# Performance work log

Hardware: AMD Instinct MI355X
Metric: run time of the kernel (lower is better)

Reference implementation:

```python
import jax, jax.numpy as jnp
import numpy as np

PATCH = 7
PAD = PATCH // 2  # 3


def _to_gray(x):
    # x: [B,3,H,W] -> [B,1,H,W]
    return 0.299 * x[:, 0:1] + 0.587 * x[:, 1:2] + 0.114 * x[:, 2:3]


def _census_transform(x):
    # x: [B,C,H,W] RGB -> grayscale, then 48 shifted binary comparisons.
    if x.shape[1] == 3:
        x = _to_gray(x)
    B, C, H, W = x.shape
    x_pad = jnp.pad(x, ((0, 0), (0, 0), (PAD, PAD), (PAD, PAD)), mode='reflect')
    center = x
    feats = []
    for i in range(PATCH):
        for j in range(PATCH):
            if i == PAD and j == PAD:
                continue
            neighbor = x_pad[:, :, i:i + H, j:j + W]
            feats.append((center > neighbor).astype(x.dtype))
    return jnp.concatenate(feats, axis=1)  # [B,48,H,W]


def setup_inputs() -> dict:
    key = jax.random.key(0)
    k1, k2 = jax.random.split(key)
    B, C, H, W = 8, 3, 512, 512
    pred = jax.random.uniform(k1, (B, C, H, W), dtype=jnp.float32)
    target = jax.random.uniform(k2, (B, C, H, W), dtype=jnp.float32)
    return {"pred": pred, "target": target}


def reference(pred, target):
    pred_census = _census_transform(pred)
    target_census = _census_transform(target)
    return jnp.abs(pred_census - target_census).mean()
```

## Files before the change

kernel.cpp:

```cpp
#include <hip/hip_runtime.h>


#define BATCH 8
#define HH 512
#define WW 512
#define PLANE (HH * WW)
#define TW 64
#define TH 32
#define LW 70
#define LH 38
#define PITCH 44
#define NTHREADS 512

__global__ __launch_bounds__(NTHREADS, 8)
void census_fused(const float* __restrict__ pred,
                  const float* __restrict__ target,
                  float* __restrict__ out) {
    __shared__ __align__(16) float sP[LW][PITCH];
    __shared__ __align__(16) float sT[LW][PITCH];

    const int b   = blockIdx.z;
    const int ty0 = blockIdx.y * TH;
    const int tx0 = blockIdx.x * TW;
    const float* __restrict__ pb = pred + (size_t)b * 3 * PLANE;
    const float* __restrict__ tb = target + (size_t)b * 3 * PLANE;

    for (int idx = threadIdx.x; idx < LW * LH; idx += NTHREADS) {
        const int ly = idx / LW;
        const int lx = idx - ly * LW;
        int gy = ty0 + ly - 3;
        int gx = tx0 + lx - 3;
        gy = gy < 0 ? -gy : (gy >= HH ? 2 * HH - 2 - gy : gy);
        gx = gx < 0 ? -gx : (gx >= WW ? 2 * WW - 2 - gx : gx);
        const int off = gy * WW + gx;
        const float p0 = pb[off], p1 = pb[off + PLANE], p2 = pb[off + 2 * PLANE];
        const float t0 = tb[off], t1 = tb[off + PLANE], t2 = tb[off + 2 * PLANE];
        sP[lx][ly] = 0.299f * p0 + 0.587f * p1 + 0.114f * p2;
        sT[lx][ly] = 0.299f * t0 + 0.587f * t1 + 0.114f * t2;
    }
    __syncthreads();

    const int c   = threadIdx.x & 63;
    const int pr0 = (threadIdx.x >> 6) * 4;

    int cnt = 0;
    float cP[4], cT[4];

    {
        const float* colP = &sP[c + 3][pr0];
        const float* colT = &sT[c + 3][pr0];
        float wP[10], wT[10];
        *(float4*)&wP[0] = *(const float4*)(colP);
        *(float4*)&wP[4] = *(const float4*)(colP + 4);
        *(float2*)&wP[8] = *(const float2*)(colP + 8);
        *(float4*)&wT[0] = *(const float4*)(colT);
        *(float4*)&wT[4] = *(const float4*)(colT + 4);
        *(float2*)&wT[8] = *(const float2*)(colT + 8);
        #pragma unroll
        for (int p = 0; p < 4; ++p) { cP[p] = wP[3 + p]; cT[p] = wT[3 + p]; }
        #pragma unroll
        for (int p = 0; p < 4; ++p) {
            #pragma unroll
            for (int dy = -3; dy <= 3; ++dy) {
                if (dy == 0) continue;
                const bool bp = cP[p] > wP[3 + p + dy];
                const bool bt = cT[p] > wT[3 + p + dy];
                cnt += (bp != bt) ? 1 : 0;
            }
        }
    }
    #pragma unroll
    for (int t = 0; t < 6; ++t) {
        const int jj = (t < 3) ? t : t + 1;
        const float* colP = &sP[c + jj][pr0];
        const float* colT = &sT[c + jj][pr0];
        float wP[10], wT[10];
        *(float4*)&wP[0] = *(const float4*)(colP);
        *(float4*)&wP[4] = *(const float4*)(colP + 4);
        *(float2*)&wP[8] = *(const float2*)(colP + 8);
        *(float4*)&wT[0] = *(const float4*)(colT);
        *(float4*)&wT[4] = *(const float4*)(colT + 4);
        *(float2*)&wT[8] = *(const float2*)(colT + 8);
        #pragma unroll
        for (int p = 0; p < 4; ++p) {
            #pragma unroll
            for (int dy = -3; dy <= 3; ++dy) {
                const bool bp = cP[p] > wP[3 + p + dy];
                const bool bt = cT[p] > wT[3 + p + dy];
                cnt += (bp != bt) ? 1 : 0;
            }
        }
    }

    #pragma unroll
    for (int o = 32; o > 0; o >>= 1) cnt += __shfl_down(cnt, o, 64);
    __shared__ int wsum[8];
    if ((threadIdx.x & 63) == 0) wsum[threadIdx.x >> 6] = cnt;
    __syncthreads();
    if (threadIdx.x == 0) {
        int tot = 0;
        #pragma unroll
        for (int w = 0; w < 8; ++w) tot += wsum[w];
        atomicAdd(out, (float)tot * (1.0f / 100663296.0f));
    }
}

extern "C" void kernel_launch(void* const* d_in, const int* in_sizes, int n_in,
                              void* d_out, int out_size, void* d_ws, size_t ws_size,
                              hipStream_t stream) {
    const float* pred   = (const float*)d_in[0];
    const float* target = (const float*)d_in[1];
    float* out = (float*)d_out;

    hipMemsetAsync(out, 0, sizeof(float), stream);

    dim3 grid(WW / TW, HH / TH, BATCH);
    census_fused<<<grid, NTHREADS, 0, stream>>>(pred, target, out);
}
```

Measured before the change: 101.3 us.

## Enlarge tiles, vectorize interior staging, overlap second-half staging with compute

Tile height doubles to 64 rows, so each thread handles an 8-row band and vertical halo overhead shrinks. Interior blocks stage the RGB planes with float4 global loads, and edge blocks keep a scalar path with reflection. Staging is split in two: the top half is loaded first, then the lower four waves load the remaining rows while the upper four waves compute their bands. This aims to hide load latency and cut halo reloads, at the cost of more registers, a lower occupancy hint and fewer blocks.

```diff
diff --git a/kernel.cpp b/kernel.cpp
--- a/kernel.cpp
+++ b/kernel.cpp
@@ -6,96 +6,136 @@
 #define WW 512
 #define PLANE (HH * WW)
 #define TW 64
-#define TH 32
-#define LW 70
-#define LH 38
-#define PITCH 44
-#define NTHREADS 512
+#define TH 64
+#define SCOLS 72
+#define HROWS 70
+#define S1 38
+#define S2 (HROWS - S1)
+#define KPR 18
+#define PITCH 76
+#define NT 512
 
-__global__ __launch_bounds__(NTHREADS, 8)
+__device__ __forceinline__ int refl(int v, int n) {
+    return v < 0 ? -v : (v >= n ? 2 * n - 2 - v : v);
+}
+
+__global__ __launch_bounds__(NT, 4)
 void census_fused(const float* __restrict__ pred,
                   const float* __restrict__ target,
                   float* __restrict__ out) {
-    __shared__ __align__(16) float sP[LW][PITCH];
-    __shared__ __align__(16) float sT[LW][PITCH];
+    __shared__ __align__(16) float sP[SCOLS][PITCH];
+    __shared__ __align__(16) float sT[SCOLS][PITCH];
 
     const int b   = blockIdx.z;
     const int ty0 = blockIdx.y * TH;
     const int tx0 = blockIdx.x * TW;
-    const float* __restrict__ pb = pred + (size_t)b * 3 * PLANE;
+    const float* __restrict__ pb = pred   + (size_t)b * 3 * PLANE;
     const float* __restrict__ tb = target + (size_t)b * 3 * PLANE;
+    const bool fastx = (blockIdx.x >= 1 && blockIdx.x <= 6);
 
-    for (int idx = threadIdx.x; idx < LW * LH; idx += NTHREADS) {
-        const int ly = idx / LW;
-        const int lx = idx - ly * LW;
-        int gy = ty0 + ly - 3;
-        int gx = tx0 + lx - 3;
-        gy = gy < 0 ? -gy : (gy >= HH ? 2 * HH - 2 - gy : gy);
-        gx = gx < 0 ? -gx : (gx >= WW ? 2 * WW - 2 - gx : gx);
+    auto stage_fast = [&](int hy, int k) {
+        const int gy  = refl(ty0 + hy - 3, HH);
+        const int off = gy * WW + tx0 - 4 + 4 * k;
+        const float4 pr = *(const float4*)(pb + off);
+        const float4 pg = *(const float4*)(pb + off + PLANE);
+        const float4 pc = *(const float4*)(pb + off + 2 * PLANE);
+        const float4 tr = *(const float4*)(tb + off);
+        const float4 tg = *(const float4*)(tb + off + PLANE);
+        const float4 tc = *(const float4*)(tb + off + 2 * PLANE);
+        const int lx = 4 * k;
+        sP[lx + 0][hy] = 0.299f * pr.x + 0.587f * pg.x + 0.114f * pc.x;
+        sP[lx + 1][hy] = 0.299f * pr.y + 0.587f * pg.y + 0.114f * pc.y;
+        sP[lx + 2][hy] = 0.299f * pr.z + 0.587f * pg.z + 0.114f * pc.z;
+        sP[lx + 3][hy] = 0.299f * pr.w + 0.587f * pg.w + 0.114f * pc.w;
+        sT[lx + 0][hy] = 0.299f * tr.x + 0.587f * tg.x + 0.114f * tc.x;
+        sT[lx + 1][hy] = 0.299f * tr.y + 0.587f * tg.y + 0.114f * tc.y;
+        sT[lx + 2][hy] = 0.299f * tr.z + 0.587f * tg.z + 0.114f * tc.z;
+        sT[lx + 3][hy] = 0.299f * tr.w + 0.587f * tg.w + 0.114f * tc.w;
+    };
+    auto stage_scalar = [&](int hy, int lx) {
+        const int gy  = refl(ty0 + hy - 3, HH);
+        const int gx  = refl(tx0 + lx - 4, WW);
         const int off = gy * WW + gx;
-        const float p0 = pb[off], p1 = pb[off + PLANE], p2 = pb[off + 2 * PLANE];
-        const float t0 = tb[off], t1 = tb[off + PLANE], t2 = tb[off + 2 * PLANE];
-        sP[lx][ly] = 0.299f * p0 + 0.587f * p1 + 0.114f * p2;
-        sT[lx][ly] = 0.299f * t0 + 0.587f * t1 + 0.114f * t2;
+        sP[lx][hy] = 0.299f * pb[off] + 0.587f * pb[off + PLANE] + 0.114f * pb[off + 2 * PLANE];
+        sT[lx][hy] = 0.299f * tb[off] + 0.587f * tb[off + PLANE] + 0.114f * tb[off + 2 * PLANE];
+    };
+
+    if (fastx) {
+        for (int idx = threadIdx.x; idx < S1 * KPR; idx += NT) {
+            const int hy = idx / KPR;
+            stage_fast(hy, idx - hy * KPR);
+        }
+    } else {
+        for (int idx = threadIdx.x; idx < S1 * SCOLS; idx += NT) {
+            const int hy = idx / SCOLS;
+            stage_scalar(hy, idx - hy * SCOLS);
+        }
     }
     __syncthreads();
 
-    const int c   = threadIdx.x & 63;
-    const int pr0 = (threadIdx.x >> 6) * 4;
+    const int wv = threadIdx.x >> 6;
+    const int c  = threadIdx.x & 63;
 
-    int cnt = 0;
-    float cP[4], cT[4];
-
-    {
-        const float* colP = &sP[c + 3][pr0];
-        const float* colT = &sT[c + 3][pr0];
-        float wP[10], wT[10];
-        *(float4*)&wP[0] = *(const float4*)(colP);
-        *(float4*)&wP[4] = *(const float4*)(colP + 4);
-        *(float2*)&wP[8] = *(const float2*)(colP + 8);
-        *(float4*)&wT[0] = *(const float4*)(colT);
-        *(float4*)&wT[4] = *(const float4*)(colT + 4);
-        *(float2*)&wT[8] = *(const float2*)(colT + 8);
+    auto load_col = [&](const float* col, float* w) {
+        *(float4*)&w[0]  = *(const float4*)(col);
+        *(float4*)&w[4]  = *(const float4*)(col + 4);
+        *(float4*)&w[8]  = *(const float4*)(col + 8);
+        *(float2*)&w[12] = *(const float2*)(col + 12);
+    };
+    auto band_count = [&](int pr0) -> int {
+        float wP[14], wT[14], cP[8], cT[8];
+        int cnt = 0;
+        load_col(&sP[c + 4][pr0], wP);
+        load_col(&sT[c + 4][pr0], wT);
         #pragma unroll
-        for (int p = 0; p < 4; ++p) { cP[p] = wP[3 + p]; cT[p] = wT[3 + p]; }
+        for (int p = 0; p < 8; ++p) { cP[p] = wP[3 + p]; cT[p] = wT[3 + p]; }
         #pragma unroll
-        for (int p = 0; p < 4; ++p) {
+        for (int p = 0; p < 8; ++p) {
             #pragma unroll
             for (int dy = -3; dy <= 3; ++dy) {
                 if (dy == 0) continue;
-                const bool bp = cP[p] > wP[3 + p + dy];
-                const bool bt = cT[p] > wT[3 + p + dy];
-                cnt += (bp != bt) ? 1 : 0;
+                cnt += ((cP[p] > wP[3 + p + dy]) != (cT[p] > wT[3 + p + dy])) ? 1 : 0;
+            }
+        }
+        #pragma unroll
+        for (int t = 0; t < 6; ++t) {
+            const int lx = c + 1 + (t < 3 ? t : t + 1);
+            load_col(&sP[lx][pr0], wP);
+            load_col(&sT[lx][pr0], wT);
+            #pragma unroll
+            for (int p = 0; p < 8; ++p) {
+                #pragma unroll
+                for (int dy = -3; dy <= 3; ++dy)
+                    cnt += ((cP[p] > wP[3 + p + dy]) != (cT[p] > wT[3 + p + dy])) ? 1 : 0;
+            }
+        }
+        return cnt;
+    };
+
+    int cnt = 0;
+    if (wv < 4) {
+        cnt = band_count(wv * 8);
+    } else {
+        const int t2 = threadIdx.x - 256;
+        if (fastx) {
+            for (int idx = t2; idx < S2 * KPR; idx += 256) {
+                const int r = idx / KPR;
+                stage_fast(S1 + r, idx - r * KPR);
+            }
+        } else {
+            for (int idx = t2; idx < S2 * SCOLS; idx += 256) {
+                const int r = idx / SCOLS;
+                stage_scalar(S1 + r, idx - r * SCOLS);
             }
         }
     }
-    #pragma unroll
-    for (int t = 0; t < 6; ++t) {
-        const int jj = (t < 3) ? t : t + 1;
-        const float* colP = &sP[c + jj][pr0];
-        const float* colT = &sT[c + jj][pr0];
-        float wP[10], wT[10];
-        *(float4*)&wP[0] = *(const float4*)(colP);
-        *(float4*)&wP[4] = *(const float4*)(colP + 4);
-        *(float2*)&wP[8] = *(const float2*)(colP + 8);
-        *(float4*)&wT[0] = *(const float4*)(colT);
-        *(float4*)&wT[4] = *(const float4*)(colT + 4);
-        *(float2*)&wT[8] = *(const float2*)(colT + 8);
-        #pragma unroll
-        for (int p = 0; p < 4; ++p) {
-            #pragma unroll
-            for (int dy = -3; dy <= 3; ++dy) {
-                const bool bp = cP[p] > wP[3 + p + dy];
-                const bool bt = cT[p] > wT[3 + p + dy];
-                cnt += (bp != bt) ? 1 : 0;
-            }
-        }
-    }
+    __syncthreads();
+    if (wv >= 4) cnt = band_count(wv * 8);
 
     #pragma unroll
     for (int o = 32; o > 0; o >>= 1) cnt += __shfl_down(cnt, o, 64);
     __shared__ int wsum[8];
-    if ((threadIdx.x & 63) == 0) wsum[threadIdx.x >> 6] = cnt;
+    if ((threadIdx.x & 63) == 0) wsum[wv] = cnt;
     __syncthreads();
     if (threadIdx.x == 0) {
         int tot = 0;
@@ -115,5 +155,5 @@
     hipMemsetAsync(out, 0, sizeof(float), stream);
 
     dim3 grid(WW / TW, HH / TH, BATCH);
-    census_fused<<<grid, NTHREADS, 0, stream>>>(pred, target, out);
+    census_fused<<<grid, NT, 0, stream>>>(pred, target, out);
 }
```

After: 113.8 us. +12.3%, slower.
